# Performance work log

Measured on AMD Instinct MI355X. Metric: run time of the kernel, lower is better.

## Reference

```python
import jax, jax.numpy as jnp
import numpy as np

EPS = 1e-6
H = 16       # query heads
KVH = 8      # kv heads
DH = 64      # head dim
HID = 1024


def _rms_norm(x, w, eps=EPS):
    ms = jnp.mean(jnp.square(x.astype(jnp.float32)), axis=-1, keepdims=True) + eps
    y = x.astype(jnp.float32) * jax.lax.rsqrt(ms)
    if w is not None:
        y = y * w.astype(jnp.float32)
    return y.astype(x.dtype)


def _rotate_half(x):
    h = x.shape[-1] // 2
    return jnp.concatenate([-x[..., h:], x[..., :h]], axis=-1)


def _multi_axis_rope(x, cos, sin, ndim):
    # x: [B,S,Hd,DH]; cos/sin: [S, rot_total]
    dh = x.shape[-1]
    rot = 2 * (dh // (2 * ndim))
    outs = []
    for i in range(ndim):
        sl = slice(i * rot, (i + 1) * rot)
        xp = x[..., sl]
        cp = cos[:, sl][:, None, :]   # [S,1,rot] broadcasts over heads
        sp = sin[:, sl][:, None, :]
        outs.append(xp * cp + _rotate_half(xp) * sp)
    return jnp.concatenate(outs, axis=-1)


def setup_inputs() -> dict:
    key = jax.random.key(0)
    ks = jax.random.split(key, 10)
    B, S = 4, 2048
    inp = {
        "hidden_states": jax.random.normal(ks[0], (B, S, HID), dtype=jnp.float32),
        "cos": jax.random.uniform(ks[1], (S, DH), dtype=jnp.float32, minval=-1.0, maxval=1.0),
        "sin": jax.random.uniform(ks[2], (S, DH), dtype=jnp.float32, minval=-1.0, maxval=1.0),
        "position_ids": jax.random.randint(ks[3], (B, S, 2), 0, 64).astype(jnp.int64),
        "attention_mask": jnp.ones((B, S), dtype=bool),
        "Wq": jax.random.normal(ks[4], (HID, H * DH), dtype=jnp.float32) * 0.02,
        "Wk": jax.random.normal(ks[5], (HID, KVH * DH), dtype=jnp.float32) * 0.02,
        "Wv": jax.random.normal(ks[6], (HID, KVH * DH), dtype=jnp.float32) * 0.02,
        "Wo": jax.random.normal(ks[7], (H * DH, HID), dtype=jnp.float32) * 0.02,
        "q_norm_w": jnp.ones((DH,), dtype=jnp.float32),
        "k_norm_w": jnp.ones((DH,), dtype=jnp.float32),
    }
    return inp


def reference(hidden_states, cos, sin, position_ids, attention_mask, Wq, Wk, Wv, Wo, q_norm_w, k_norm_w):
    B, S, _ = hidden_states.shape
    ndim = int(position_ids.shape[-1])

    q = (hidden_states @ Wq).reshape(B, S, H, DH)
    k = (hidden_states @ Wk).reshape(B, S, KVH, DH)
    v = (hidden_states @ Wv).reshape(B, S, KVH, DH)

    q = _rms_norm(q, q_norm_w)
    k = _rms_norm(k, k_norm_w)
    v = _rms_norm(v, None)  # v_norm has no scale

    q = _multi_axis_rope(q, cos, sin, ndim)
    k = _multi_axis_rope(k, cos, sin, ndim)

    # [B, heads, S, DH]; repeat kv heads for GQA
    q = q.transpose(0, 2, 1, 3)
    k = jnp.repeat(k.transpose(0, 2, 1, 3), H // KVH, axis=1)
    v = jnp.repeat(v.transpose(0, 2, 1, 3), H // KVH, axis=1)

    scores = jnp.einsum("bhqd,bhkd->bhqk", q, k)  # scaling = 1.0
    key_mask = attention_mask[:, None, None, :]
    scores = jnp.where(key_mask, scores, jnp.finfo(scores.dtype).min)
    probs = jax.nn.softmax(scores.astype(jnp.float32), axis=-1).astype(v.dtype)

    out = jnp.einsum("bhqk,bhkd->bhqd", probs, v)
    out = out.transpose(0, 2, 1, 3).reshape(B, S, H * DH)
    out = jnp.where(attention_mask[:, :, None], out, 0.0)
    return out @ Wo
```

## Files before the change

kernel.cpp:

```cpp
#include <hip/hip_runtime.h>
#include <stdint.h>
#include <stddef.h>

typedef unsigned short u16;
typedef unsigned int   u32;
typedef unsigned short u16x8 __attribute__((ext_vector_type(8)));
typedef __attribute__((ext_vector_type(8))) __bf16 bf16x8;
typedef __attribute__((ext_vector_type(4))) float f32x4;

__device__ __forceinline__ float bf2f(u16 v){
  union { unsigned u; float f; } x; x.u = ((unsigned)v) << 16; return x.f;
}
__device__ __forceinline__ u16 f2bf(float f){
  union { float f; unsigned u; } x; x.f = f;
  return (u16)((x.u + 0x7fffu + ((x.u >> 16) & 1u)) >> 16);
}

__device__ __forceinline__ float exp2_fast(float x){
  float r; asm("v_exp_f32 %0, %1" : "=v"(r) : "v"(x)); return r;
}
__device__ __forceinline__ u32 cvt_pk_bf16(float lo, float hi){
  u32 r; asm("v_cvt_pk_bf16_f32 %0, %1, %2" : "=v"(r) : "v"(lo), "v"(hi)); return r;
}

__device__ __forceinline__ f32x4 mfma16(bf16x8 a, bf16x8 b, f32x4 c){
  return __builtin_amdgcn_mfma_f32_16x16x32_bf16(a, b, c, 0, 0, 0);
}

#define AS1 __attribute__((address_space(1)))
#define AS3 __attribute__((address_space(3)))
__device__ __forceinline__ void gload_lds16(const void* g, void* l){
  __builtin_amdgcn_global_load_lds((const AS1 void*)g, (AS3 void*)l, 16, 0, 0);
}

__global__ void f32_to_bf16(const float* __restrict__ in, u16* __restrict__ out,
                            int n4){
  for (size_t i = blockIdx.x * blockDim.x + threadIdx.x; i < (size_t)n4;
       i += (size_t)gridDim.x * blockDim.x){
    float4 v = *(const float4*)(in + i * 4);
    ushort4 o = { f2bf(v.x), f2bf(v.y), f2bf(v.z), f2bf(v.w) };
    *(ushort4*)(out + i * 4) = o;
  }
}

__global__ void conv_transpose(const float* __restrict__ in, u16* __restrict__ out,
                               int R, int C){
  __shared__ float t[32][33];
  int c0 = blockIdx.x * 32, r0 = blockIdx.y * 32;
  int tx = threadIdx.x, ty = threadIdx.y;
  t[ty][tx] = in[(size_t)(r0 + ty) * C + c0 + tx];
  __syncthreads();
  out[(size_t)(c0 + ty) * R + r0 + tx] = f2bf(t[tx][ty]);
}

#define BM 128
#define BN 128
#define BK 32

__device__ __forceinline__ void stage_gemm(const u16* __restrict__ A,
                                           const u16* __restrict__ Bt, int K,
                                           int m0, int n0, int k0,
                                           u16* Albuf, u16* Blbuf,
                                           int wid, int lane){
  int rl = lane >> 2, cl = (lane & 3) * 8;
#pragma unroll
  for (int j = 0; j < 2; j++){
    int row = wid * 32 + j * 16 + rl;
    gload_lds16(A  + (size_t)(m0 + row) * K + k0 + cl, Albuf + wid * 1024 + j * 512);
    gload_lds16(Bt + (size_t)(n0 + row) * K + k0 + cl, Blbuf + wid * 1024 + j * 512);
  }
}

template<bool F32OUT>
__global__ __launch_bounds__(256, 2)
void gemm_bt(const u16* __restrict__ A, const u16* __restrict__ Bt,
             void* __restrict__ Cv, int M, int N, int K){
  __shared__ __align__(16) u16 Al[2][BM * BK];
  __shared__ __align__(16) u16 Bl[2][BN * BK];
  const int tid = threadIdx.x;
  const int wid = tid >> 6, lane = tid & 63;
  const int g = lane >> 4, col = lane & 15;
  const int wr = wid >> 1, wc = wid & 1;

  int nb  = gridDim.x * gridDim.y;
  int lid = blockIdx.y * gridDim.x + blockIdx.x;
  int cpx = nb >> 3;
  int sid = (lid & 7) * cpx + (lid >> 3);
  int bx  = sid % gridDim.x, by = sid / gridDim.x;
  const int m0 = by * BM, n0 = bx * BN;

  f32x4 acc[4][4];
#pragma unroll
  for (int i = 0; i < 4; i++)
#pragma unroll
    for (int j = 0; j < 4; j++) acc[i][j] = (f32x4){0.f, 0.f, 0.f, 0.f};

  stage_gemm(A, Bt, K, m0, n0, 0, &Al[0][0], &Bl[0][0], wid, lane);
  __syncthreads();

  const int KT = K / BK;
  int buf = 0;
  for (int kt = 0; kt < KT; ++kt){
    if (kt + 1 < KT)
      stage_gemm(A, Bt, K, m0, n0, (kt + 1) * BK, &Al[buf ^ 1][0], &Bl[buf ^ 1][0], wid, lane);

    bf16x8 af[4], bfv[4];
#pragma unroll
    for (int i = 0; i < 4; i++){
      af[i]  = *(const bf16x8*)&Al[buf][(wr * 64 + i * 16 + col) * BK + g * 8];
      bfv[i] = *(const bf16x8*)&Bl[buf][(wc * 64 + i * 16 + col) * BK + g * 8];
    }
#pragma unroll
    for (int mi = 0; mi < 4; mi++)
#pragma unroll
      for (int ni = 0; ni < 4; ni++)
        acc[mi][ni] = mfma16(af[mi], bfv[ni], acc[mi][ni]);

    __syncthreads();
    buf ^= 1;
  }

#pragma unroll
  for (int mi = 0; mi < 4; mi++)
#pragma unroll
    for (int ni = 0; ni < 4; ni++)
#pragma unroll
      for (int r = 0; r < 4; r++){
        int row = m0 + wr * 64 + mi * 16 + g * 4 + r;
        int cc  = n0 + wc * 64 + ni * 16 + col;
        if (F32OUT) ((float*)Cv)[(size_t)row * N + cc] = acc[mi][ni][r];
        else        ((u16*)Cv)[(size_t)row * N + cc] = f2bf(acc[mi][ni][r]);
      }
}

__global__ void prep_q(const u16* __restrict__ qkv, u16* __restrict__ Qn,
                       const float* __restrict__ cosb, const float* __restrict__ sinb,
                       const float* __restrict__ w){
  int gid = blockIdx.x * 4 + (threadIdx.x >> 6);
  int lane = threadIdx.x & 63;
  int s = gid & 2047;
  int bh = gid >> 11;
  int h = bh & 15, b = bh >> 4;
  float x = bf2f(qkv[((size_t)(b * 2048 + s)) * 2048 + h * 64 + lane]);
  float ss = x * x;
#pragma unroll
  for (int off = 32; off >= 1; off >>= 1) ss += __shfl_xor(ss, off, 64);
  float y = x * rsqrtf(ss * (1.f / 64.f) + 1e-6f);
  y *= w[lane];
  float yp = __shfl_xor(y, 16, 64);
  float rot = (lane & 16) ? yp : -yp;
  Qn[(size_t)gid * 64 + lane] = f2bf(y * cosb[s * 64 + lane] + rot * sinb[s * 64 + lane]);
}

__global__ void prep_k(const u16* __restrict__ qkv, u16* __restrict__ Kn,
                       const float* __restrict__ cosb, const float* __restrict__ sinb,
                       const float* __restrict__ w){
  int gid = blockIdx.x * 4 + (threadIdx.x >> 6);
  int lane = threadIdx.x & 63;
  int s = gid & 2047;
  int bk = gid >> 11;
  int kvh = bk & 7, b = bk >> 3;
  float x = bf2f(qkv[((size_t)(b * 2048 + s)) * 2048 + 1024 + kvh * 64 + lane]);
  float ss = x * x;
#pragma unroll
  for (int off = 32; off >= 1; off >>= 1) ss += __shfl_xor(ss, off, 64);
  float y = x * rsqrtf(ss * (1.f / 64.f) + 1e-6f);
  y *= w[lane];
  float yp = __shfl_xor(y, 16, 64);
  float rot = (lane & 16) ? yp : -yp;
  int swz = ((((lane >> 3) ^ s) & 7) << 3) | (lane & 7);
  Kn[(size_t)gid * 64 + swz] = f2bf(y * cosb[s * 64 + lane] + rot * sinb[s * 64 + lane]);
}

__global__ __launch_bounds__(256)
void prep_v(const u16* __restrict__ qkv, u16* __restrict__ Vn){
  int blk = blockIdx.x;
  int stile = blk & 31, kvh = (blk >> 5) & 7, b = blk >> 8;
  int wid = threadIdx.x >> 6, lane = threadIdx.x & 63;
  __shared__ u16 T[64][68];
#pragma unroll 4
  for (int j = 0; j < 16; j++){
    int sl = wid * 16 + j;
    int s = stile * 64 + sl;
    float x = bf2f(qkv[((size_t)(b * 2048 + s)) * 2048 + 1536 + kvh * 64 + lane]);
    float ss = x * x;
#pragma unroll
    for (int off = 32; off >= 1; off >>= 1) ss += __shfl_xor(ss, off, 64);
    T[sl][lane] = f2bf(x * rsqrtf(ss * (1.f / 64.f) + 1e-6f));
  }
  __syncthreads();
  size_t obase = ((size_t)(b * 8 + kvh) * 64) * 2048 + stile * 64;
#pragma unroll
  for (int it = 0; it < 2; it++){
    int t = it * 256 + threadIdx.x;
    int d = t >> 3, c = t & 7;
    int cl = c ^ (d & 7);
    u16x8 v;
#pragma unroll
    for (int i = 0; i < 8; i++) v[i] = T[cl * 8 + i][d];
    *(u16x8*)(Vn + obase + (size_t)d * 2048 + c * 8) = v;
  }
}

__global__ __launch_bounds__(256, 2)
void flash_attn(const u16* __restrict__ Qn, const u16* __restrict__ Kn,
                const u16* __restrict__ Vn, u16* __restrict__ AO){
  const int S = 2048;
  const float L2E = 1.4426950408889634f;
  const float C2 = 30.f;
  const int b = blockIdx.z, h = blockIdx.y, qt = blockIdx.x;
  const int kvh = h >> 1;
  const int wid = threadIdx.x >> 6, lane = threadIdx.x & 63;
  const int g = lane >> 4, col = lane & 15;
  const int q0 = qt * 256 + wid * 64;

  __shared__ __align__(16) u16 Klds[2][64 * 64];
  __shared__ __align__(16) u16 Vlds[2][64 * 64];
  __shared__ __align__(16) u16 Plds[4][16 * 64];

  bf16x8 ones;
#pragma unroll
  for (int i = 0; i < 8; i++) ones[i] = (__bf16)1.0f;

  bf16x8 aq[4][2];
#pragma unroll
  for (int cg = 0; cg < 4; cg++){
    const u16* qp = Qn + ((size_t)((b * 16 + h) * S) + q0 + cg * 16 + col) * 64;
    aq[cg][0] = *(const bf16x8*)(qp + g * 8);
    aq[cg][1] = *(const bf16x8*)(qp + 32 + g * 8);
  }

  const u16* Kbase = Kn + (size_t)(b * 8 + kvh) * S * 64;
  const u16* Vbase = Vn + (size_t)(b * 8 + kvh) * 64 * S;

  f32x4 acc[4][4];
  f32x4 lacc[4];
#pragma unroll
  for (int cg = 0; cg < 4; cg++){
    lacc[cg] = (f32x4){0.f, 0.f, 0.f, 0.f};
#pragma unroll
    for (int i = 0; i < 4; i++) acc[cg][i] = (f32x4){0.f, 0.f, 0.f, 0.f};
  }

  const int sw = col & 7;
  const int pswz = sw << 4;
  char* Pw = (char*)&Plds[wid][0];

  auto STAGE = [&](int bi, int kt){
    int kc0 = kt * 64;
#pragma unroll
    for (int cc = 0; cc < 2; cc++){
      int chunk = cc * 4 + wid;
      gload_lds16(Kbase + (size_t)kc0 * 64 + chunk * 512 + lane * 8,
                  &Klds[bi][chunk * 512]);
      int drow = chunk * 8 + (lane >> 3);
      gload_lds16(Vbase + (size_t)drow * S + kc0 + (lane & 7) * 8,
                  &Vlds[bi][chunk * 512]);
    }
  };

  int buf = 0;
  STAGE(0, 0);
  __syncthreads();

  for (int kt = 0; kt < S / 64; ++kt){
    if (kt + 1 < S / 64) STAGE(buf ^ 1, kt + 1);

    const u16* Kb = &Klds[buf][0];
    const u16* Vb = &Vlds[buf][0];

    bf16x8 kf[4][2], vf[4][2];
#pragma unroll
    for (int c = 0; c < 4; c++){
      const u16* kb = Kb + (c * 16 + col) * 64;
      kf[c][0] = *(const bf16x8*)(kb + (g ^ sw) * 8);
      kf[c][1] = *(const bf16x8*)(kb + ((4 + g) ^ sw) * 8);
      const u16* vb = Vb + (c * 16 + col) * 64;
      vf[c][0] = *(const bf16x8*)(vb + (g ^ sw) * 8);
      vf[c][1] = *(const bf16x8*)(vb + ((4 + g) ^ sw) * 8);
    }

#pragma unroll
    for (int cg = 0; cg < 4; cg++){
      f32x4 sf[4];
      __builtin_amdgcn_s_setprio(1);
#pragma unroll
      for (int c = 0; c < 4; c++){
        f32x4 z = (f32x4){0.f, 0.f, 0.f, 0.f};
        z = mfma16(kf[c][0], aq[cg][0], z);
        sf[c] = mfma16(kf[c][1], aq[cg][1], z);
      }
      __builtin_amdgcn_s_setprio(0);

#pragma unroll
      for (int c = 0; c < 4; c++){
        float p0 = exp2_fast(__builtin_fmaf(sf[c][0], L2E, -C2));
        float p1 = exp2_fast(__builtin_fmaf(sf[c][1], L2E, -C2));
        float p2 = exp2_fast(__builtin_fmaf(sf[c][2], L2E, -C2));
        float p3 = exp2_fast(__builtin_fmaf(sf[c][3], L2E, -C2));
        uint2 pw;
        pw.x = cvt_pk_bf16(p0, p1);
        pw.y = cvt_pk_bf16(p2, p3);
        *(uint2*)(Pw + ((col * 128 + c * 32 + g * 8) ^ pswz)) = pw;
      }

      bf16x8 pf0 = *(const bf16x8*)(Pw + ((col * 128 + g * 16) ^ pswz));
      bf16x8 pf1 = *(const bf16x8*)(Pw + ((col * 128 + 64 + g * 16) ^ pswz));
      __builtin_amdgcn_s_setprio(1);
#pragma unroll
      for (int cd = 0; cd < 4; cd++){
        acc[cg][cd] = mfma16(vf[cd][0], pf0, acc[cg][cd]);
        acc[cg][cd] = mfma16(vf[cd][1], pf1, acc[cg][cd]);
      }
      lacc[cg] = mfma16(ones, pf0, lacc[cg]);
      lacc[cg] = mfma16(ones, pf1, lacc[cg]);
      __builtin_amdgcn_s_setprio(0);
    }

    __syncthreads();
    buf ^= 1;
  }

#pragma unroll
  for (int cg = 0; cg < 4; cg++){
    float linv = 1.f / lacc[cg][0];
#pragma unroll
    for (int cd = 0; cd < 4; cd++){
      uint2 o;
      o.x = cvt_pk_bf16(acc[cg][cd][0] * linv, acc[cg][cd][1] * linv);
      o.y = cvt_pk_bf16(acc[cg][cd][2] * linv, acc[cg][cd][3] * linv);
      *(uint2*)(AO + ((size_t)((b * S + q0 + cg * 16 + col) * 16 + h)) * 64
                + cd * 16 + g * 4) = o;
    }
  }
}

extern "C" void kernel_launch(void* const* d_in, const int* in_sizes, int n_in,
                              void* d_out, int out_size, void* d_ws, size_t ws_size,
                              hipStream_t stream){
  const int Btok = 8192;
  const float* hs   = (const float*)d_in[0];
  const float* cosb = (const float*)d_in[1];
  const float* sinb = (const float*)d_in[2];
  const float* Wq = (const float*)d_in[5];
  const float* Wk = (const float*)d_in[6];
  const float* Wv = (const float*)d_in[7];
  const float* Wo = (const float*)d_in[8];
  const float* qw = (const float*)d_in[9];
  const float* kw = (const float*)d_in[10];
  float* out = (float*)d_out;

  char* ws = (char*)d_ws;
  u16* hsB   = (u16*)ws;               ws += (size_t)Btok * 1024 * 2;
  u16* WqkvT = (u16*)ws;               ws += (size_t)2048 * 1024 * 2;
  u16* WoT   = (u16*)ws;               ws += (size_t)1024 * 1024 * 2;
  u16* QKV   = (u16*)ws;               ws += (size_t)Btok * 2048 * 2;
  u16* Qn    = (u16*)ws;               ws += (size_t)Btok * 1024 * 2;
  u16* Kn    = (u16*)ws;               ws += (size_t)Btok * 512  * 2;
  u16* Vn    = (u16*)ws;               ws += (size_t)Btok * 512  * 2;
  u16* AO    = hsB;

  f32_to_bf16<<<2048, 256, 0, stream>>>(hs, hsB, Btok * 1024 / 4);

  dim3 tb(32, 32);
  conv_transpose<<<dim3(32, 32), tb, 0, stream>>>(Wq, WqkvT,              1024, 1024);
  conv_transpose<<<dim3(16, 32), tb, 0, stream>>>(Wk, WqkvT + 1024 * 1024, 1024, 512);
  conv_transpose<<<dim3(16, 32), tb, 0, stream>>>(Wv, WqkvT + 1536 * 1024, 1024, 512);
  conv_transpose<<<dim3(32, 32), tb, 0, stream>>>(Wo, WoT,                1024, 1024);

  gemm_bt<false><<<dim3(16, 64), 256, 0, stream>>>(hsB, WqkvT, QKV, Btok, 2048, 1024);

  prep_q<<<32768, 256, 0, stream>>>(QKV, Qn, cosb, sinb, qw);
  prep_k<<<16384, 256, 0, stream>>>(QKV, Kn, cosb, sinb, kw);
  prep_v<<<1024, 256, 0, stream>>>(QKV, Vn);

  flash_attn<<<dim3(8, 16, 4), 256, 0, stream>>>(Qn, Kn, Vn, AO);

  gemm_bt<true><<<dim3(8, 64), 256, 0, stream>>>(AO, WoT, out, Btok, 1024, 1024);
}
```

Before: 201.3 us.

## Replace GEMM with 256x128 triple-buffered swizzled-LDS kernel and pre-swizzled operands

```diff
diff --git a/kernel.cpp b/kernel.cpp
--- a/kernel.cpp
+++ b/kernel.cpp
@@ -33,101 +33,138 @@
   __builtin_amdgcn_global_load_lds((const AS1 void*)g, (AS3 void*)l, 16, 0, 0);
 }
 
-__global__ void f32_to_bf16(const float* __restrict__ in, u16* __restrict__ out,
-                            int n4){
-  for (size_t i = blockIdx.x * blockDim.x + threadIdx.x; i < (size_t)n4;
-       i += (size_t)gridDim.x * blockDim.x){
-    float4 v = *(const float4*)(in + i * 4);
-    ushort4 o = { f2bf(v.x), f2bf(v.y), f2bf(v.z), f2bf(v.w) };
-    *(ushort4*)(out + i * 4) = o;
-  }
-}
-
-__global__ void conv_transpose(const float* __restrict__ in, u16* __restrict__ out,
-                               int R, int C){
+__global__ void f32_to_bf16_swz(const float* __restrict__ in, u16* __restrict__ out,
+                                int total_chunks){
+  for (int i = blockIdx.x * blockDim.x + threadIdx.x; i < total_chunks;
+       i += gridDim.x * blockDim.x){
+    int row = i >> 7, c = i & 127;
+    int cs = (c & ~7) | ((c & 7) ^ (row & 7));
+    const float* p = in + ((size_t)i << 3);
+    float4 v0 = *(const float4*)p;
+    float4 v1 = *(const float4*)(p + 4);
+    u16x8 o = { f2bf(v0.x), f2bf(v0.y), f2bf(v0.z), f2bf(v0.w),
+                f2bf(v1.x), f2bf(v1.y), f2bf(v1.z), f2bf(v1.w) };
+    *(u16x8*)(out + (((size_t)row << 7) + cs) * 8) = o;
+  }
+}
+
+__global__ void conv_transpose_swz(const float* __restrict__ in, u16* __restrict__ out,
+                                   int R, int C){
   __shared__ float t[32][33];
   int c0 = blockIdx.x * 32, r0 = blockIdx.y * 32;
   int tx = threadIdx.x, ty = threadIdx.y;
   t[ty][tx] = in[(size_t)(r0 + ty) * C + c0 + tx];
   __syncthreads();
-  out[(size_t)(c0 + ty) * R + r0 + tx] = f2bf(t[tx][ty]);
-}
-
-#define BM 128
-#define BN 128
-#define BK 32
-
-__device__ __forceinline__ void stage_gemm(const u16* __restrict__ A,
-                                           const u16* __restrict__ Bt, int K,
-                                           int m0, int n0, int k0,
-                                           u16* Albuf, u16* Blbuf,
-                                           int wid, int lane){
-  int rl = lane >> 2, cl = (lane & 3) * 8;
-#pragma unroll
-  for (int j = 0; j < 2; j++){
-    int row = wid * 32 + j * 16 + rl;
-    gload_lds16(A  + (size_t)(m0 + row) * K + k0 + cl, Albuf + wid * 1024 + j * 512);
-    gload_lds16(Bt + (size_t)(n0 + row) * K + k0 + cl, Blbuf + wid * 1024 + j * 512);
+  int tid = ty * 32 + tx;
+  if (tid < 128){
+    int orow = tid >> 2, oc = tid & 3;
+    int gr = c0 + orow;
+    int gc = (r0 >> 3) + oc;
+    int gcs = (gc & ~7) | ((gc & 7) ^ (gr & 7));
+    u16x8 v;
+#pragma unroll
+    for (int i = 0; i < 8; i++) v[i] = f2bf(t[oc * 8 + i][orow]);
+    *(u16x8*)(out + (size_t)gr * R + gcs * 8) = v;
   }
 }
 
 template<bool F32OUT>
-__global__ __launch_bounds__(256, 2)
-void gemm_bt(const u16* __restrict__ A, const u16* __restrict__ Bt,
-             void* __restrict__ Cv, int M, int N, int K){
-  __shared__ __align__(16) u16 Al[2][BM * BK];
-  __shared__ __align__(16) u16 Bl[2][BN * BK];
+__global__ __launch_bounds__(512, 2)
+void gemm8(const u16* __restrict__ A, const u16* __restrict__ Bt,
+           void* __restrict__ Cv, int M, int N, int K){
+  __shared__ __align__(16) u16 Ab[3][256 * 64];
+  __shared__ __align__(16) u16 Bb[3][128 * 64];
   const int tid = threadIdx.x;
   const int wid = tid >> 6, lane = tid & 63;
   const int g = lane >> 4, col = lane & 15;
-  const int wr = wid >> 1, wc = wid & 1;
+  const int wr = wid >> 2, wcn = wid & 3;
 
   int nb  = gridDim.x * gridDim.y;
   int lid = blockIdx.y * gridDim.x + blockIdx.x;
   int cpx = nb >> 3;
   int sid = (lid & 7) * cpx + (lid >> 3);
   int bx  = sid % gridDim.x, by = sid / gridDim.x;
-  const int m0 = by * BM, n0 = bx * BN;
-
-  f32x4 acc[4][4];
-#pragma unroll
-  for (int i = 0; i < 4; i++)
-#pragma unroll
-    for (int j = 0; j < 4; j++) acc[i][j] = (f32x4){0.f, 0.f, 0.f, 0.f};
-
-  stage_gemm(A, Bt, K, m0, n0, 0, &Al[0][0], &Bl[0][0], wid, lane);
-  __syncthreads();
-
-  const int KT = K / BK;
-  int buf = 0;
-  for (int kt = 0; kt < KT; ++kt){
-    if (kt + 1 < KT)
-      stage_gemm(A, Bt, K, m0, n0, (kt + 1) * BK, &Al[buf ^ 1][0], &Bl[buf ^ 1][0], wid, lane);
-
-    bf16x8 af[4], bfv[4];
-#pragma unroll
-    for (int i = 0; i < 4; i++){
-      af[i]  = *(const bf16x8*)&Al[buf][(wr * 64 + i * 16 + col) * BK + g * 8];
-      bfv[i] = *(const bf16x8*)&Bl[buf][(wc * 64 + i * 16 + col) * BK + g * 8];
-    }
-#pragma unroll
-    for (int mi = 0; mi < 4; mi++)
-#pragma unroll
-      for (int ni = 0; ni < 4; ni++)
-        acc[mi][ni] = mfma16(af[mi], bfv[ni], acc[mi][ni]);
-
-    __syncthreads();
-    buf ^= 1;
-  }
-
-#pragma unroll
-  for (int mi = 0; mi < 4; mi++)
-#pragma unroll
-    for (int ni = 0; ni < 4; ni++)
+  const int m0 = by * 256, n0 = bx * 128;
+
+  f32x4 acc[8][2];
+#pragma unroll
+  for (int i = 0; i < 8; i++)
+#pragma unroll
+    for (int j = 0; j < 2; j++) acc[i][j] = (f32x4){0.f, 0.f, 0.f, 0.f};
+
+  const int srow = wid * 8 + (lane >> 3);
+  const int scl  = (lane & 7) * 8;
+  const int swz  = col & 7;
+
+  auto STAGE = [&](int bi, int k0){
+#pragma unroll
+    for (int j = 0; j < 4; j++)
+      gload_lds16(A + (size_t)(m0 + j * 64 + srow) * K + k0 + scl,
+                  &Ab[bi][j * 4096 + wid * 512]);
+#pragma unroll
+    for (int j = 0; j < 2; j++)
+      gload_lds16(Bt + (size_t)(n0 + j * 64 + srow) * K + k0 + scl,
+                  &Bb[bi][j * 4096 + wid * 512]);
+  };
+
+  const int NT = K / 64;
+  STAGE(0, 0);
+  STAGE(1, 64);
+  asm volatile("s_waitcnt vmcnt(6)");
+  __builtin_amdgcn_sched_barrier(0);
+  __builtin_amdgcn_s_barrier();
+  __builtin_amdgcn_sched_barrier(0);
+
+  int cb = 0, sb = 2;
+  for (int t = 0; t < NT; ++t){
+    if (t + 2 < NT) STAGE(sb, (t + 2) * 64);
+
+    bf16x8 bfr[2][2];
+#pragma unroll
+    for (int ni = 0; ni < 2; ni++){
+      int row = wcn * 32 + ni * 16 + col;
+#pragma unroll
+      for (int ks = 0; ks < 2; ks++)
+        bfr[ni][ks] = *(const bf16x8*)&Bb[cb][row * 64 + (((ks * 4 + g) ^ swz) << 3)];
+    }
+#pragma unroll
+    for (int q = 0; q < 4; q++){
+      bf16x8 afr[2][2];
+#pragma unroll
+      for (int m2 = 0; m2 < 2; m2++){
+        int row = wr * 128 + q * 32 + m2 * 16 + col;
+#pragma unroll
+        for (int ks = 0; ks < 2; ks++)
+          afr[m2][ks] = *(const bf16x8*)&Ab[cb][row * 64 + (((ks * 4 + g) ^ swz) << 3)];
+      }
+      __builtin_amdgcn_s_setprio(1);
+#pragma unroll
+      for (int m2 = 0; m2 < 2; m2++)
+#pragma unroll
+        for (int ni = 0; ni < 2; ni++)
+#pragma unroll
+          for (int ks = 0; ks < 2; ks++)
+            acc[q * 2 + m2][ni] = mfma16(afr[m2][ks], bfr[ni][ks], acc[q * 2 + m2][ni]);
+      __builtin_amdgcn_s_setprio(0);
+    }
+
+    if (t + 2 < NT) asm volatile("s_waitcnt vmcnt(6)");
+    else            asm volatile("s_waitcnt vmcnt(0)");
+    __builtin_amdgcn_sched_barrier(0);
+    __builtin_amdgcn_s_barrier();
+    __builtin_amdgcn_sched_barrier(0);
+    cb = (cb == 2) ? 0 : cb + 1;
+    sb = (sb == 2) ? 0 : sb + 1;
+  }
+
+#pragma unroll
+  for (int mi = 0; mi < 8; mi++)
+#pragma unroll
+    for (int ni = 0; ni < 2; ni++)
 #pragma unroll
       for (int r = 0; r < 4; r++){
-        int row = m0 + wr * 64 + mi * 16 + g * 4 + r;
-        int cc  = n0 + wc * 64 + ni * 16 + col;
+        int row = m0 + wr * 128 + mi * 16 + g * 4 + r;
+        int cc  = n0 + wcn * 32 + ni * 16 + col;
         if (F32OUT) ((float*)Cv)[(size_t)row * N + cc] = acc[mi][ni][r];
         else        ((u16*)Cv)[(size_t)row * N + cc] = f2bf(acc[mi][ni][r]);
       }
@@ -324,13 +361,14 @@
 #pragma unroll
   for (int cg = 0; cg < 4; cg++){
     float linv = 1.f / lacc[cg][0];
+    int s = q0 + cg * 16 + col;
 #pragma unroll
     for (int cd = 0; cd < 4; cd++){
       uint2 o;
       o.x = cvt_pk_bf16(acc[cg][cd][0] * linv, acc[cg][cd][1] * linv);
       o.y = cvt_pk_bf16(acc[cg][cd][2] * linv, acc[cg][cd][3] * linv);
-      *(uint2*)(AO + ((size_t)((b * S + q0 + cg * 16 + col) * 16 + h)) * 64
-                + cd * 16 + g * 4) = o;
+      int pc = (cd * 2 + (g >> 1)) ^ sw;
+      *(uint2*)(AO + (size_t)(b * S + s) * 1024 + h * 64 + pc * 8 + (g & 1) * 4) = o;
     }
   }
 }
@@ -360,15 +398,15 @@
   u16* Vn    = (u16*)ws;               ws += (size_t)Btok * 512  * 2;
   u16* AO    = hsB;
 
-  f32_to_bf16<<<2048, 256, 0, stream>>>(hs, hsB, Btok * 1024 / 4);
+  f32_to_bf16_swz<<<2048, 256, 0, stream>>>(hs, hsB, Btok * 128);
 
   dim3 tb(32, 32);
-  conv_transpose<<<dim3(32, 32), tb, 0, stream>>>(Wq, WqkvT,              1024, 1024);
-  conv_transpose<<<dim3(16, 32), tb, 0, stream>>>(Wk, WqkvT + 1024 * 1024, 1024, 512);
-  conv_transpose<<<dim3(16, 32), tb, 0, stream>>>(Wv, WqkvT + 1536 * 1024, 1024, 512);
-  conv_transpose<<<dim3(32, 32), tb, 0, stream>>>(Wo, WoT,                1024, 1024);
-
-  gemm_bt<false><<<dim3(16, 64), 256, 0, stream>>>(hsB, WqkvT, QKV, Btok, 2048, 1024);
+  conv_transpose_swz<<<dim3(32, 32), tb, 0, stream>>>(Wq, WqkvT,               1024, 1024);
+  conv_transpose_swz<<<dim3(16, 32), tb, 0, stream>>>(Wk, WqkvT + 1024 * 1024, 1024, 512);
+  conv_transpose_swz<<<dim3(16, 32), tb, 0, stream>>>(Wv, WqkvT + 1536 * 1024, 1024, 512);
+  conv_transpose_swz<<<dim3(32, 32), tb, 0, stream>>>(Wo, WoT,                 1024, 1024);
+
+  gemm8<false><<<dim3(16, 32), 512, 0, stream>>>(hsB, WqkvT, QKV, Btok, 2048, 1024);
 
   prep_q<<<32768, 256, 0, stream>>>(QKV, Qn, cosb, sinb, qw);
   prep_k<<<16384, 256, 0, stream>>>(QKV, Kn, cosb, sinb, kw);
@@ -376,5 +414,5 @@
 
   flash_attn<<<dim3(8, 16, 4), 256, 0, stream>>>(Qn, Kn, Vn, AO);
 
-  gemm_bt<true><<<dim3(8, 64), 256, 0, stream>>>(AO, WoT, out, Btok, 1024, 1024);
-}
+  gemm8<true><<<dim3(8, 32), 512, 0, stream>>>(AO, WoT, out, Btok, 1024, 1024);
+}
```

Measured after the change: 213.0 us. 5.8% more time.
